# Kernel tuning notes

Hardware: AMD Instinct MI355X
Metric: run time of the kernel (lower is better)

The kernel has to match this reference:

```python
import jax, jax.numpy as jnp
import numpy as np

ORDER = 16
FRAME = 160


def setup_inputs() -> dict:
    key = jax.random.key(0)
    x = jax.random.normal(key, (32, 160000, 1), dtype=jnp.float32)
    return {"x": x}


def _lpc_residual(x):
    # x: [B, T, 1] -> residual [B, T, 1]
    B, T, _ = x.shape
    fs, order = FRAME, ORDER
    nf = T // fs
    frames = x[..., 0].reshape(B * nf, fs)  # [N, fs], N = B*nf

    # autocorrelation lags 0..order: r[n, j] = sum_t frames[n, t] * frames[n, t+j]
    r = jnp.stack(
        [jnp.sum(frames[:, : fs - j] * frames[:, j:], axis=1) for j in range(order + 1)],
        axis=1,
    )  # [N, order+1]

    N = frames.shape[0]
    a = jnp.zeros((N, order + 1), frames.dtype).at[:, 0].set(1.0)
    e = r[:, 0]
    # Levinson-Durbin recursion (exact sign convention of the source module)
    for i in range(1, order + 1):
        acc = r[:, i] - jnp.sum(a[:, 1:i] * r[:, 1:i][:, ::-1], axis=1)
        k = acc / e
        a = a.at[:, 1:i].add(-k[:, None] * a[:, i - 1:0:-1])
        a = a.at[:, i].set(k)
        e = e * (1.0 - k * k)

    # FIR: res[n, t] = sum_{j=0..order} a[n, j] * frames[n, t-j]  (lfilter(a, [1], frm))
    padded = jnp.pad(frames, ((0, 0), (order, 0)))
    shifted = jnp.stack(
        [padded[:, order - j: order - j + fs] for j in range(order + 1)], axis=1
    )  # [N, order+1, fs]
    res = jnp.einsum('nj,njt->nt', a, shifted)
    return res.reshape(B, T, 1)


def reference(x):
    return _lpc_residual(x)
```

## Files before the change

### kernel.cpp

```cpp
#include <hip/hip_runtime.h>


#define FS 160
#define ORD 16
#define LPF 8
#define FPW 8
#define WPB 4
#define FPB (FPW * WPB)
#define SLOT 196
#define CHUNK 20

__global__ __launch_bounds__(256) void lpc_kernel(const float* __restrict__ x,
                                                  float* __restrict__ out,
                                                  int nframes) {
    __shared__ float sf[WPB * FPW * SLOT];
    const int tid = threadIdx.x;
    const int wv = tid >> 6;
    const int lane = tid & 63;
    const int g = lane >> 3;
    const int li = lane & 7;
    const int wframe0 = (blockIdx.x * WPB + wv) * FPW;
    if (wframe0 >= nframes) return;
    float* s = sf + wv * FPW * SLOT;

    const float4* xin = (const float4*)(x + (size_t)wframe0 * FS);
#pragma unroll
    for (int c = 0; c < 5; ++c) {
        int i = lane + 64 * c;
        int gfo = 4 * i;
        int f = gfo / FS;
        int p = gfo - f * FS;
        float4 v = xin[i];
        *(float4*)(s + f * SLOT + 16 + p) = v;
    }
#pragma unroll
    for (int c = 0; c < 4; ++c) {
        int z = lane + 64 * c;
        int f = z >> 5;
        int q = z & 31;
        int off = (q < 16) ? q : (q + 160);
        s[f * SLOT + off] = 0.0f;
    }
    __syncthreads();

    const float* fb = s + g * SLOT;

    float w[36];
    {
        const float* wa = fb + 16 + CHUNK * li;
#pragma unroll
        for (int m = 0; m < 36; m += 4)
            *(float4*)(w + m) = *(const float4*)(wa + m);
    }
    float r[ORD + 1];
#pragma unroll
    for (int j = 0; j <= ORD; ++j) {
        float p = 0.0f;
#pragma unroll
        for (int m = 0; m < CHUNK; ++m) p = fmaf(w[m], w[m + j], p);
        r[j] = p;
    }
#pragma unroll
    for (int off = 4; off >= 1; off >>= 1) {
#pragma unroll
        for (int j = 0; j <= ORD; ++j) r[j] += __shfl_xor(r[j], off, 64);
    }

    float a[ORD + 1], tmp[ORD + 1];
    a[0] = 1.0f;
#pragma unroll
    for (int j = 1; j <= ORD; ++j) a[j] = 0.0f;
    float e = r[0];
#pragma unroll
    for (int i = 1; i <= ORD; ++i) {
        float acc = r[i];
#pragma unroll
        for (int m = 1; m < i; ++m) acc -= a[m] * r[i - m];
        float k = acc * __builtin_amdgcn_rcpf(e);
#pragma unroll
        for (int m = 1; m < i; ++m) tmp[m] = a[m] - k * a[i - m];
#pragma unroll
        for (int m = 1; m < i; ++m) a[m] = tmp[m];
        a[i] = k;
        e *= (1.0f - k * k);
    }

    float v[36];
    {
        const float* wf = fb + CHUNK * li;
#pragma unroll
        for (int m = 0; m < 36; m += 4)
            *(float4*)(v + m) = *(const float4*)(wf + m);
    }
    float4* ob = (float4*)(out + (size_t)(wframe0 + g) * FS + CHUNK * li);
#pragma unroll
    for (int q = 0; q < 5; ++q) {
        float4 o;
#pragma unroll
        for (int u = 0; u < 4; ++u) {
            int m = 4 * q + u;
            float acc2 = 0.0f;
#pragma unroll
            for (int j = 0; j <= ORD; ++j) acc2 = fmaf(a[j], v[16 + m - j], acc2);
            ((float*)&o)[u] = acc2;
        }
        ob[q] = o;
    }
}

extern "C" void kernel_launch(void* const* d_in, const int* in_sizes, int n_in,
                              void* d_out, int out_size, void* d_ws, size_t ws_size,
                              hipStream_t stream) {
    const float* x = (const float*)d_in[0];
    float* out = (float*)d_out;
    const int total = in_sizes[0];
    const int nframes = total / FS;
    const int blocks = (nframes + FPB - 1) / FPB;
    lpc_kernel<<<blocks, 256, 0, stream>>>(x, out, nframes);
}
```

Baseline: 18.61 us.

## Spread each frame over 16 lanes and reduce autocorrelation with DPP row rotates

Halves frames per wave and the per-lane chunk, so 16 lanes cooperate on each frame instead of 8. The grid doubles, and per-lane register arrays shrink to float2 vectors. The cross-lane autocorrelation reduction moves from __shfl_xor to DPP row-rotate adds. The block-wide __syncthreads is dropped, since each wave only touches its own LDS region. The Levinson inner product is split into two FMA chains, and occupancy is hinted via launch bounds. The trade-off is that the serial Levinson recursion is now repeated redundantly by twice as many lanes.

```diff
diff --git a/kernel.cpp b/kernel.cpp
--- a/kernel.cpp
+++ b/kernel.cpp
@@ -1,69 +1,74 @@
 #include <hip/hip_runtime.h>
 
 
+typedef float f32x2 __attribute__((ext_vector_type(2)));
+
 #define FS 160
 #define ORD 16
-#define LPF 8
-#define FPW 8
+#define FPW 4
 #define WPB 4
 #define FPB (FPW * WPB)
 #define SLOT 196
-#define CHUNK 20
+#define CHUNK 10
 
-__global__ __launch_bounds__(256) void lpc_kernel(const float* __restrict__ x,
-                                                  float* __restrict__ out,
-                                                  int nframes) {
+template <int CTRL>
+__device__ __forceinline__ float rotadd(float v) {
+    int p = __builtin_amdgcn_update_dpp(0, __builtin_bit_cast(int, v),
+                                        CTRL, 0xF, 0xF, false);
+    return v + __builtin_bit_cast(float, p);
+}
+
+__global__ __launch_bounds__(256, 6) void lpc_kernel(const float* __restrict__ x,
+                                                     float* __restrict__ out,
+                                                     int nframes) {
     __shared__ float sf[WPB * FPW * SLOT];
     const int tid = threadIdx.x;
     const int wv = tid >> 6;
     const int lane = tid & 63;
-    const int g = lane >> 3;
-    const int li = lane & 7;
+    const int g = lane >> 4;
+    const int li = lane & 15;
     const int wframe0 = (blockIdx.x * WPB + wv) * FPW;
     if (wframe0 >= nframes) return;
     float* s = sf + wv * FPW * SLOT;
 
     const float4* xin = (const float4*)(x + (size_t)wframe0 * FS);
 #pragma unroll
-    for (int c = 0; c < 5; ++c) {
-        int i = lane + 64 * c;
-        int gfo = 4 * i;
-        int f = gfo / FS;
-        int p = gfo - f * FS;
-        float4 v = xin[i];
-        *(float4*)(s + f * SLOT + 16 + p) = v;
+    for (int c = 0; c < 3; ++c) {
+        unsigned i = (unsigned)lane + 64u * c;
+        if (c < 2 || i < 160u) {
+            float4 v = xin[i];
+            unsigned f = i / 40u;
+            unsigned p = 4u * i - f * 160u;
+            *(float4*)(s + f * SLOT + 16 + p) = v;
+        }
     }
 #pragma unroll
-    for (int c = 0; c < 4; ++c) {
+    for (int c = 0; c < 2; ++c) {
         int z = lane + 64 * c;
-        int f = z >> 5;
-        int q = z & 31;
-        int off = (q < 16) ? q : (q + 160);
-        s[f * SLOT + off] = 0.0f;
+        int f = z >> 5, q = z & 31;
+        s[f * SLOT + (q < 16 ? q : q + 160)] = 0.0f;
     }
-    __syncthreads();
 
     const float* fb = s + g * SLOT;
 
-    float w[36];
+    f32x2 w2[13];
     {
         const float* wa = fb + 16 + CHUNK * li;
 #pragma unroll
-        for (int m = 0; m < 36; m += 4)
-            *(float4*)(w + m) = *(const float4*)(wa + m);
+        for (int m = 0; m < 13; ++m) w2[m] = *(const f32x2*)(wa + 2 * m);
     }
+#define W(m) (w2[(m) >> 1][(m) & 1])
     float r[ORD + 1];
 #pragma unroll
     for (int j = 0; j <= ORD; ++j) {
         float p = 0.0f;
 #pragma unroll
-        for (int m = 0; m < CHUNK; ++m) p = fmaf(w[m], w[m + j], p);
+        for (int m = 0; m < CHUNK; ++m) p = fmaf(W(m), W(m + j), p);
+        p = rotadd<0x121>(p);
+        p = rotadd<0x122>(p);
+        p = rotadd<0x124>(p);
+        p = rotadd<0x128>(p);
         r[j] = p;
-    }
-#pragma unroll
-    for (int off = 4; off >= 1; off >>= 1) {
-#pragma unroll
-        for (int j = 0; j <= ORD; ++j) r[j] += __shfl_xor(r[j], off, 64);
     }
 
     float a[ORD + 1], tmp[ORD + 1];
@@ -73,38 +78,41 @@
     float e = r[0];
 #pragma unroll
     for (int i = 1; i <= ORD; ++i) {
-        float acc = r[i];
+        float s0 = 0.0f, s1 = 0.0f;
 #pragma unroll
-        for (int m = 1; m < i; ++m) acc -= a[m] * r[i - m];
-        float k = acc * __builtin_amdgcn_rcpf(e);
+        for (int m = 1; m < i; ++m) {
+            if (m & 1) s0 = fmaf(a[m], r[i - m], s0);
+            else       s1 = fmaf(a[m], r[i - m], s1);
+        }
+        float k = (r[i] - s0 - s1) * __builtin_amdgcn_rcpf(e);
 #pragma unroll
-        for (int m = 1; m < i; ++m) tmp[m] = a[m] - k * a[i - m];
+        for (int m = 1; m < i; ++m) tmp[m] = fmaf(-k, a[i - m], a[m]);
 #pragma unroll
         for (int m = 1; m < i; ++m) a[m] = tmp[m];
         a[i] = k;
-        e *= (1.0f - k * k);
+        e = e * (1.0f - k * k);
     }
 
-    float v[36];
+    f32x2 v2[13];
     {
-        const float* wf = fb + CHUNK * li;
+        const float* vb = fb + CHUNK * li;
 #pragma unroll
-        for (int m = 0; m < 36; m += 4)
-            *(float4*)(v + m) = *(const float4*)(wf + m);
+        for (int m = 0; m < 13; ++m) v2[m] = *(const f32x2*)(vb + 2 * m);
     }
-    float4* ob = (float4*)(out + (size_t)(wframe0 + g) * FS + CHUNK * li);
+#define V(m) (v2[(m) >> 1][(m) & 1])
+    float* op = out + (size_t)(wframe0 + g) * FS + CHUNK * li;
 #pragma unroll
     for (int q = 0; q < 5; ++q) {
-        float4 o;
+        f32x2 o;
 #pragma unroll
-        for (int u = 0; u < 4; ++u) {
-            int m = 4 * q + u;
-            float acc2 = 0.0f;
+        for (int u = 0; u < 2; ++u) {
+            int t = 2 * q + u;
+            float acc = 0.0f;
 #pragma unroll
-            for (int j = 0; j <= ORD; ++j) acc2 = fmaf(a[j], v[16 + m - j], acc2);
-            ((float*)&o)[u] = acc2;
+            for (int j = 0; j <= ORD; ++j) acc = fmaf(a[j], V(16 + t - j), acc);
+            o[u] = acc;
         }
-        ob[q] = o;
+        *(f32x2*)(op + 2 * q) = o;
     }
 }
 
```

New measurement: 18.89 us. About the same (+1.5%).
